# Performance work log

Hardware: AMD Instinct MI355X
Metric: run time of the kernel (lower is better)

Reference implementation:

```python
import jax, jax.numpy as jnp
import numpy as np

N = 50000
E = 800000
F_IN = 128
HID = 128
OUT = 64
EPS = 1e-5


def gcn_conv(x, src, dst, deg_inv_sqrt, W, b):
    # h = x @ W  (dense transform first, like PyG GCNConv)
    h = x @ W  # [N, F_out]
    norm = deg_inv_sqrt[src] * deg_inv_sqrt[dst]  # [E+N] (self-loops included)
    msgs = norm[:, None] * h[src]  # gather + scale, [E+N, F_out]
    out = jax.ops.segment_sum(msgs, dst, num_segments=N)  # scatter-add to targets
    return out + b


def setup_inputs() -> dict:
    key = jax.random.key(0)
    ks = jax.random.split(key, 9)
    x = jax.random.normal(ks[0], (N, F_IN), dtype=jnp.float32)
    edge_index = jax.random.randint(ks[1], (2, E), 0, N, dtype=jnp.int64)
    s = 1.0 / np.sqrt(F_IN)
    W1 = jax.random.uniform(ks[2], (F_IN, HID), jnp.float32, -s, s)
    b1 = jnp.zeros((HID,), jnp.float32)
    sh = 1.0 / np.sqrt(HID)
    Wmu = jax.random.uniform(ks[3], (HID, OUT), jnp.float32, -sh, sh)
    bmu = jnp.zeros((OUT,), jnp.float32)
    Wlv = jax.random.uniform(ks[4], (HID, OUT), jnp.float32, -sh, sh)
    blv = jnp.zeros((OUT,), jnp.float32)
    gamma = jnp.ones((HID,), jnp.float32)
    beta = jnp.zeros((HID,), jnp.float32)
    return {"x": x, "edge_index": edge_index, "W1": W1, "b1": b1,
            "gamma": gamma, "beta": beta, "Wmu": Wmu, "bmu": bmu,
            "Wlv": Wlv, "blv": blv}


def reference(x, edge_index, W1, b1, gamma, beta, Wmu, bmu, Wlv, blv):
    # Add self-loops (GCNConv default) and compute symmetric normalization once.
    loop = jnp.arange(N, dtype=edge_index.dtype)
    src = jnp.concatenate([edge_index[0], loop])
    dst = jnp.concatenate([edge_index[1], loop])
    deg = jax.ops.segment_sum(jnp.ones_like(dst, dtype=x.dtype), dst, num_segments=N)
    deg_inv_sqrt = jnp.where(deg > 0, jax.lax.rsqrt(deg), 0.0)

    h = jax.nn.relu(gcn_conv(x, src, dst, deg_inv_sqrt, W1, b1))
    # per-node LayerNorm over feature dim
    mean = jnp.mean(h, axis=-1, keepdims=True)
    var = jnp.var(h, axis=-1, keepdims=True)
    h = (h - mean) * jax.lax.rsqrt(var + EPS) * gamma + beta

    mu = gcn_conv(h, src, dst, deg_inv_sqrt, Wmu, bmu)
    logvar = gcn_conv(h, src, dst, deg_inv_sqrt, Wlv, blv)
    return mu, logvar
```

## Files before the change

### kernel.cpp

```cpp
#include <hip/hip_runtime.h>

#define NN 50000
#define EE 800000
#define FF 128
#define OO 64
#define EPSF 1e-5f
#define SCB 196
#define EBLK 3125
#define GBLK 391

typedef unsigned int uint;
typedef unsigned short ushort;
typedef __attribute__((ext_vector_type(8))) short short8;
typedef __attribute__((ext_vector_type(4))) float f32x4;

__device__ __forceinline__ float bflo(uint v) { return __uint_as_float(v << 16); }
__device__ __forceinline__ float bfhi(uint v) { return __uint_as_float(v & 0xFFFF0000u); }
__device__ __forceinline__ uint f2bf(float f) {
  uint b = __float_as_uint(f);
  return (b + 0x7FFFu + ((b >> 16) & 1u)) >> 16;
}
__device__ __forceinline__ uint pack2(float x, float y) { return f2bf(x) | (f2bf(y) << 16); }

__device__ __forceinline__ int eidx(const void* ei, long long pos, int f64) {
  if (f64) return (int)((const long long*)ei)[pos];
  return ((const int*)ei)[pos];
}

__global__ void k_init(const void* ei, int* flag, int* cnt) {
  int i = blockIdx.x * 256 + threadIdx.x;
  if (i < NN) cnt[i] = 0;
  if (i == 0) {
    const int* p = (const int*)ei;
    int any = 0;
    for (int j = 1; j < 128; j += 2) any |= p[j];
    *flag = (any == 0) ? 1 : 0;
  }
}

__global__ void k_deg_rank(const void* ei, const int* __restrict__ flag,
                           int* __restrict__ cnt, int* __restrict__ rank) {
  int e = blockIdx.x * 256 + threadIdx.x;
  if (e >= EE) return;
  int f64 = *flag;
  int d = eidx(ei, (long long)EE + e, f64);
  rank[e] = atomicAdd(&cnt[d], 1);
}

__global__ __launch_bounds__(256) void k_dis_part(const int* __restrict__ cnt,
                                                  float* __restrict__ dis,
                                                  int* __restrict__ bsum) {
  int i = blockIdx.x * 256 + threadIdx.x;
  int v = (i < NN) ? cnt[i] : 0;
  if (i < NN) dis[i] = rsqrtf((float)(v + 1));
  int s = v;
#pragma unroll
  for (int m = 1; m < 64; m <<= 1) s += __shfl_xor(s, m);
  __shared__ int ws[4];
  if ((threadIdx.x & 63) == 0) ws[threadIdx.x >> 6] = s;
  __syncthreads();
  if (threadIdx.x == 0) bsum[blockIdx.x] = ws[0] + ws[1] + ws[2] + ws[3];
}

__global__ __launch_bounds__(256) void k_scan_tops(const int* __restrict__ bsum,
                                                   int* __restrict__ boff,
                                                   int* __restrict__ rowptr) {
  __shared__ int s[256];
  int tid = threadIdx.x;
  int v = (tid < SCB) ? bsum[tid] : 0;
  s[tid] = v;
  __syncthreads();
  for (int off = 1; off < 256; off <<= 1) {
    int t = (tid >= off) ? s[tid - off] : 0;
    __syncthreads();
    s[tid] += t;
    __syncthreads();
  }
  if (tid < SCB) boff[tid] = s[tid] - v;
  if (tid == 255) rowptr[NN] = s[255];
}

__global__ __launch_bounds__(256) void k_scan_write(const int* __restrict__ cnt,
                                                    const int* __restrict__ boff,
                                                    int* __restrict__ rowptr) {
  int blk = blockIdx.x, tid = threadIdx.x;
  int i = blk * 256 + tid;
  int v = (i < NN) ? cnt[i] : 0;
  int lane = tid & 63, wid = tid >> 6;
  int inc = v;
#pragma unroll
  for (int off = 1; off < 64; off <<= 1) {
    int t = __shfl_up(inc, off);
    if (lane >= off) inc += t;
  }
  __shared__ int wsum[4];
  if (lane == 63) wsum[wid] = inc;
  __syncthreads();
  int wadd = 0;
  for (int wj = 0; wj < wid; ++wj) wadd += wsum[wj];
  int exc = inc - v + wadd + boff[blk];
  if (i < NN) rowptr[i] = exc;
}

__global__ void k_scatter(const void* ei, const int* __restrict__ flag,
                          const float* __restrict__ dis,
                          const int* __restrict__ rowptr,
                          const int* __restrict__ rank,
                          int2* __restrict__ cw) {
  int e = blockIdx.x * 256 + threadIdx.x;
  if (e >= EE) return;
  int f64 = *flag;
  int s = eidx(ei, e, f64);
  int d = eidx(ei, (long long)EE + e, f64);
  int p = rowptr[d] + rank[e];
  int2 v;
  v.x = s;
  v.y = __float_as_int(dis[s] * dis[d]);
  cw[p] = v;
}

__device__ __forceinline__ int wt_idx(int c, int k) {
  return c * 128 + (k ^ ((c & 7) << 3));
}

__global__ __launch_bounds__(256) void k_gemm1(const float* __restrict__ X,
                                               const float* __restrict__ W,
                                               ushort* __restrict__ T) {
  __shared__ ushort Wt[FF * FF];
  for (int i = threadIdx.x; i < FF * FF; i += 256) {
    int k = i >> 7, c = i & 127;
    Wt[wt_idx(c, k)] = (ushort)f2bf(W[i]);
  }
  __syncthreads();
  int l = threadIdx.x & 63, wv = threadIdx.x >> 6;
  int rbase = blockIdx.x * 128 + wv * 32;
  int lr = l & 15, lk = (l >> 4) << 3;
  f32x4 acc[2][8] = {};
#pragma unroll
  for (int kb = 0; kb < 4; ++kb) {
    int kk = kb * 32 + lk;
    short8 a[2];
#pragma unroll
    for (int rt = 0; rt < 2; ++rt) {
      int row = min(rbase + rt * 16 + lr, NN - 1);
      const float4* ap = (const float4*)(X + (size_t)row * FF + kk);
      float4 x0 = ap[0], x1 = ap[1];
      a[rt][0] = (short)f2bf(x0.x); a[rt][1] = (short)f2bf(x0.y);
      a[rt][2] = (short)f2bf(x0.z); a[rt][3] = (short)f2bf(x0.w);
      a[rt][4] = (short)f2bf(x1.x); a[rt][5] = (short)f2bf(x1.y);
      a[rt][6] = (short)f2bf(x1.z); a[rt][7] = (short)f2bf(x1.w);
    }
#pragma unroll
    for (int ct = 0; ct < 8; ++ct) {
      int c = ct * 16 + lr;
      short8 b = *(const short8*)&Wt[wt_idx(c, kk)];
      acc[0][ct] = __builtin_amdgcn_mfma_f32_16x16x32_bf16(a[0], b, acc[0][ct], 0, 0, 0);
      acc[1][ct] = __builtin_amdgcn_mfma_f32_16x16x32_bf16(a[1], b, acc[1][ct], 0, 0, 0);
    }
  }
  int rl = (l >> 4) * 4;
#pragma unroll
  for (int rt = 0; rt < 2; ++rt)
#pragma unroll
    for (int reg = 0; reg < 4; ++reg) {
      int row = rbase + rt * 16 + rl + reg;
      if (row < NN) {
#pragma unroll
        for (int ct = 0; ct < 8; ++ct)
          T[(size_t)row * FF + ct * 16 + lr] = (ushort)f2bf(acc[rt][ct][reg]);
      }
    }
}

__global__ __launch_bounds__(256) void k_gemm2(const ushort* __restrict__ A,
                                               const float* __restrict__ Wmu,
                                               const float* __restrict__ bmu,
                                               const float* __restrict__ Wlv,
                                               const float* __restrict__ blv,
                                               float* __restrict__ out) {
  __shared__ ushort Wt[FF * FF];
  __shared__ float sb[FF];
  for (int i = threadIdx.x; i < FF * FF; i += 256) {
    int k = i >> 7, c = i & 127;
    float v = (c < OO) ? Wmu[k * OO + c] : Wlv[k * OO + (c - OO)];
    Wt[wt_idx(c, k)] = (ushort)f2bf(v);
  }
  if (threadIdx.x < FF)
    sb[threadIdx.x] = (threadIdx.x < OO) ? bmu[threadIdx.x] : blv[threadIdx.x - OO];
  __syncthreads();
  int l = threadIdx.x & 63, wv = threadIdx.x >> 6;
  int rbase = blockIdx.x * 128 + wv * 32;
  int lr = l & 15, lk = (l >> 4) << 3;
  f32x4 acc[2][8] = {};
#pragma unroll
  for (int kb = 0; kb < 4; ++kb) {
    int kk = kb * 32 + lk;
    short8 a[2];
#pragma unroll
    for (int rt = 0; rt < 2; ++rt) {
      int row = min(rbase + rt * 16 + lr, NN - 1);
      a[rt] = *(const short8*)(A + (size_t)row * FF + kk);
    }
#pragma unroll
    for (int ct = 0; ct < 8; ++ct) {
      int c = ct * 16 + lr;
      short8 b = *(const short8*)&Wt[wt_idx(c, kk)];
      acc[0][ct] = __builtin_amdgcn_mfma_f32_16x16x32_bf16(a[0], b, acc[0][ct], 0, 0, 0);
      acc[1][ct] = __builtin_amdgcn_mfma_f32_16x16x32_bf16(a[1], b, acc[1][ct], 0, 0, 0);
    }
  }
  int rl = (l >> 4) * 4;
#pragma unroll
  for (int rt = 0; rt < 2; ++rt)
#pragma unroll
    for (int reg = 0; reg < 4; ++reg) {
      int row = rbase + rt * 16 + rl + reg;
      if (row < NN) {
#pragma unroll
        for (int ct = 0; ct < 8; ++ct) {
          int c = ct * 16 + lr;
          float v = acc[rt][ct][reg] + sb[c];
          if (ct < 4) out[(size_t)row * OO + c] = v;
          else out[(size_t)NN * OO + (size_t)row * OO + (c - OO)] = v;
        }
      }
    }
}

template <int LN>
__global__ __launch_bounds__(256) void k_gather(const int* __restrict__ rowptr,
                                                const int2* __restrict__ cw,
                                                const float* __restrict__ dis,
                                                const ushort* __restrict__ feat,
                                                const float* __restrict__ b1,
                                                const float* __restrict__ gamma,
                                                const float* __restrict__ beta,
                                                ushort* __restrict__ outp) {
  int gw = (blockIdx.x * 256 + threadIdx.x) >> 6;
  int nw = (gridDim.x * 256) >> 6;
  int lane = threadIdx.x & 63;
  for (int node = gw; node < NN; node += nw) {
    float di = dis[node];
    float sw = di * di;
    uint sv = ((const uint*)(feat + ((size_t)node << 7)))[lane];
    float ax = sw * bflo(sv), ay = sw * bfhi(sv);
    int e = rowptr[node], end = rowptr[node + 1];
    while (end - e >= 16) {
      int2 c[16];
      uint v[16];
#pragma unroll
      for (int j = 0; j < 16; ++j) c[j] = cw[e + j];
#pragma unroll
      for (int j = 0; j < 16; ++j) v[j] = ((const uint*)(feat + ((size_t)c[j].x << 7)))[lane];
#pragma unroll
      for (int j = 0; j < 16; ++j) {
        float wj = __int_as_float(c[j].y);
        ax = fmaf(wj, bflo(v[j]), ax); ay = fmaf(wj, bfhi(v[j]), ay);
      }
      e += 16;
    }
    if (end - e >= 8) {
      int2 c[8];
      uint v[8];
#pragma unroll
      for (int j = 0; j < 8; ++j) c[j] = cw[e + j];
#pragma unroll
      for (int j = 0; j < 8; ++j) v[j] = ((const uint*)(feat + ((size_t)c[j].x << 7)))[lane];
#pragma unroll
      for (int j = 0; j < 8; ++j) {
        float wj = __int_as_float(c[j].y);
        ax = fmaf(wj, bflo(v[j]), ax); ay = fmaf(wj, bfhi(v[j]), ay);
      }
      e += 8;
    }
    if (end - e >= 4) {
      int2 c[4];
      uint v[4];
#pragma unroll
      for (int j = 0; j < 4; ++j) c[j] = cw[e + j];
#pragma unroll
      for (int j = 0; j < 4; ++j) v[j] = ((const uint*)(feat + ((size_t)c[j].x << 7)))[lane];
#pragma unroll
      for (int j = 0; j < 4; ++j) {
        float wj = __int_as_float(c[j].y);
        ax = fmaf(wj, bflo(v[j]), ax); ay = fmaf(wj, bfhi(v[j]), ay);
      }
      e += 4;
    }
    for (; e < end; ++e) {
      int2 c0 = cw[e];
      uint v0 = ((const uint*)(feat + ((size_t)c0.x << 7)))[lane];
      float w0 = __int_as_float(c0.y);
      ax = fmaf(w0, bflo(v0), ax); ay = fmaf(w0, bfhi(v0), ay);
    }
    float ox, oy;
    if (LN) {
      float b0 = b1[2 * lane], b1v = b1[2 * lane + 1];
      float a0 = fmaxf(ax + b0, 0.f);
      float a1 = fmaxf(ay + b1v, 0.f);
      float s = a0 + a1, sq = a0 * a0 + a1 * a1;
#pragma unroll
      for (int m = 1; m < 64; m <<= 1) {
        s += __shfl_xor(s, m);
        sq += __shfl_xor(sq, m);
      }
      float mean = s * (1.f / 128.f);
      float var = sq * (1.f / 128.f) - mean * mean;
      float rstd = rsqrtf(var + EPSF);
      float g0 = gamma[2 * lane], g1 = gamma[2 * lane + 1];
      float be0 = beta[2 * lane], be1 = beta[2 * lane + 1];
      ox = (a0 - mean) * rstd * g0 + be0;
      oy = (a1 - mean) * rstd * g1 + be1;
    } else {
      ox = ax; oy = ay;
    }
    ((uint*)(outp + ((size_t)node << 7)))[lane] = pack2(ox, oy);
  }
}

extern "C" void kernel_launch(void* const* d_in, const int* in_sizes, int n_in,
                              void* d_out, int out_size, void* d_ws, size_t ws_size,
                              hipStream_t stream) {
  const float* x     = (const float*)d_in[0];
  const void*  ei    = d_in[1];
  const float* W1    = (const float*)d_in[2];
  const float* b1    = (const float*)d_in[3];
  const float* gamma = (const float*)d_in[4];
  const float* beta  = (const float*)d_in[5];
  const float* Wmu   = (const float*)d_in[6];
  const float* bmu   = (const float*)d_in[7];
  const float* Wlv   = (const float*)d_in[8];
  const float* blv   = (const float*)d_in[9];
  float* out = (float*)d_out;

  int*   flag   = (int*)d_ws;
  int*   cnt    = flag + 64;
  int*   rowptr = cnt + NN;
  float* dis    = (float*)(rowptr + (NN + 16));
  int*   bsum   = (int*)(dis + NN);
  int*   boff   = bsum + 256;
  int*   rank   = boff + 256;
  size_t off32  = (size_t)(64 + NN + (NN + 16) + NN + 256 + 256 + EE);
  off32 = (off32 + 63) & ~(size_t)63;
  int2*  cw     = (int2*)((int*)d_ws + off32);
  ushort* t  = (ushort*)(cw + EE);
  ushort* h  = t + (size_t)NN * FF;
  ushort* t2 = h + (size_t)NN * FF;

  k_init<<<SCB, 256, 0, stream>>>(ei, flag, cnt);
  k_deg_rank<<<EBLK, 256, 0, stream>>>(ei, flag, cnt, rank);
  k_dis_part<<<SCB, 256, 0, stream>>>(cnt, dis, bsum);
  k_scan_tops<<<1, 256, 0, stream>>>(bsum, boff, rowptr);
  k_scan_write<<<SCB, 256, 0, stream>>>(cnt, boff, rowptr);
  k_scatter<<<EBLK, 256, 0, stream>>>(ei, flag, dis, rowptr, rank, cw);

  k_gemm1<<<GBLK, 256, 0, stream>>>(x, W1, t);
  k_gather<1><<<2048, 256, 0, stream>>>(rowptr, cw, dis, t, b1, gamma, beta, h);
  k_gather<0><<<2048, 256, 0, stream>>>(rowptr, cw, dis, h, b1, gamma, beta, t2);
  k_gemm2<<<GBLK, 256, 0, stream>>>(t2, Wmu, bmu, Wlv, blv, out);
}
```

Baseline: 178.5 us.

## Split each wavefront into four edge groups with 16-byte feature loads in gather

The gather kernel now gives each wavefront one node and splits its 64 lanes into four groups of 16. Each group handles a different edge and each lane loads 16 bytes (8 bf16 features), so the per-edge rows come in as wide vector loads and several edges are in flight at once. The partial sums are combined across groups with cross-lane shuffles. The LayerNorm reduction now runs within 16 lanes, and the launch becomes one node per wave with no grid-stride loop. The cost is extra shuffle work, 8 accumulators per lane, and only two edges per group per iteration instead of the old 16-deep unroll.

New measurement: 165.9 us. 1.08x faster.

```diff
diff --git a/kernel.cpp b/kernel.cpp
--- a/kernel.cpp
+++ b/kernel.cpp
@@ -236,85 +236,95 @@
                                                 const float* __restrict__ gamma,
                                                 const float* __restrict__ beta,
                                                 ushort* __restrict__ outp) {
-  int gw = (blockIdx.x * 256 + threadIdx.x) >> 6;
-  int nw = (gridDim.x * 256) >> 6;
-  int lane = threadIdx.x & 63;
-  for (int node = gw; node < NN; node += nw) {
+  int node = blockIdx.x * 4 + (threadIdx.x >> 6);
+  if (node >= NN) return;
+  int l = threadIdx.x & 63;
+  int g = l >> 4;
+  int c16 = l & 15;
+
+  float acc[8] = {};
+  int e0 = rowptr[node], nE = rowptr[node + 1] - e0;
+  int base = 0;
+  for (; base + 8 <= nE; base += 8) {
+    int2 cA = cw[e0 + base + g];
+    int2 cB = cw[e0 + base + 4 + g];
+    uint4 vA = ((const uint4*)(feat + ((size_t)cA.x << 7)))[c16];
+    uint4 vB = ((const uint4*)(feat + ((size_t)cB.x << 7)))[c16];
+    float wA = __int_as_float(cA.y), wB = __int_as_float(cB.y);
+    acc[0] = fmaf(wA, bflo(vA.x), acc[0]); acc[1] = fmaf(wA, bfhi(vA.x), acc[1]);
+    acc[2] = fmaf(wA, bflo(vA.y), acc[2]); acc[3] = fmaf(wA, bfhi(vA.y), acc[3]);
+    acc[4] = fmaf(wA, bflo(vA.z), acc[4]); acc[5] = fmaf(wA, bfhi(vA.z), acc[5]);
+    acc[6] = fmaf(wA, bflo(vA.w), acc[6]); acc[7] = fmaf(wA, bfhi(vA.w), acc[7]);
+    acc[0] = fmaf(wB, bflo(vB.x), acc[0]); acc[1] = fmaf(wB, bfhi(vB.x), acc[1]);
+    acc[2] = fmaf(wB, bflo(vB.y), acc[2]); acc[3] = fmaf(wB, bfhi(vB.y), acc[3]);
+    acc[4] = fmaf(wB, bflo(vB.z), acc[4]); acc[5] = fmaf(wB, bfhi(vB.z), acc[5]);
+    acc[6] = fmaf(wB, bflo(vB.w), acc[6]); acc[7] = fmaf(wB, bfhi(vB.w), acc[7]);
+  }
+#pragma unroll
+  for (int t = 0; t < 2; ++t) {
+    int idx = base + t * 4 + g;
+    if (idx < nE) {
+      int2 c0 = cw[e0 + idx];
+      uint4 v = ((const uint4*)(feat + ((size_t)c0.x << 7)))[c16];
+      float w0 = __int_as_float(c0.y);
+      acc[0] = fmaf(w0, bflo(v.x), acc[0]); acc[1] = fmaf(w0, bfhi(v.x), acc[1]);
+      acc[2] = fmaf(w0, bflo(v.y), acc[2]); acc[3] = fmaf(w0, bfhi(v.y), acc[3]);
+      acc[4] = fmaf(w0, bflo(v.z), acc[4]); acc[5] = fmaf(w0, bfhi(v.z), acc[5]);
+      acc[6] = fmaf(w0, bflo(v.w), acc[6]); acc[7] = fmaf(w0, bfhi(v.w), acc[7]);
+    }
+  }
+#pragma unroll
+  for (int j = 0; j < 8; ++j) {
+    acc[j] += __shfl_xor(acc[j], 16);
+    acc[j] += __shfl_xor(acc[j], 32);
+  }
+  {
     float di = dis[node];
     float sw = di * di;
-    uint sv = ((const uint*)(feat + ((size_t)node << 7)))[lane];
-    float ax = sw * bflo(sv), ay = sw * bfhi(sv);
-    int e = rowptr[node], end = rowptr[node + 1];
-    while (end - e >= 16) {
-      int2 c[16];
-      uint v[16];
-#pragma unroll
-      for (int j = 0; j < 16; ++j) c[j] = cw[e + j];
-#pragma unroll
-      for (int j = 0; j < 16; ++j) v[j] = ((const uint*)(feat + ((size_t)c[j].x << 7)))[lane];
-#pragma unroll
-      for (int j = 0; j < 16; ++j) {
-        float wj = __int_as_float(c[j].y);
-        ax = fmaf(wj, bflo(v[j]), ax); ay = fmaf(wj, bfhi(v[j]), ay);
-      }
-      e += 16;
-    }
-    if (end - e >= 8) {
-      int2 c[8];
-      uint v[8];
-#pragma unroll
-      for (int j = 0; j < 8; ++j) c[j] = cw[e + j];
-#pragma unroll
-      for (int j = 0; j < 8; ++j) v[j] = ((const uint*)(feat + ((size_t)c[j].x << 7)))[lane];
-#pragma unroll
-      for (int j = 0; j < 8; ++j) {
-        float wj = __int_as_float(c[j].y);
-        ax = fmaf(wj, bflo(v[j]), ax); ay = fmaf(wj, bfhi(v[j]), ay);
-      }
-      e += 8;
-    }
-    if (end - e >= 4) {
-      int2 c[4];
-      uint v[4];
-#pragma unroll
-      for (int j = 0; j < 4; ++j) c[j] = cw[e + j];
-#pragma unroll
-      for (int j = 0; j < 4; ++j) v[j] = ((const uint*)(feat + ((size_t)c[j].x << 7)))[lane];
-#pragma unroll
-      for (int j = 0; j < 4; ++j) {
-        float wj = __int_as_float(c[j].y);
-        ax = fmaf(wj, bflo(v[j]), ax); ay = fmaf(wj, bfhi(v[j]), ay);
-      }
-      e += 4;
-    }
-    for (; e < end; ++e) {
-      int2 c0 = cw[e];
-      uint v0 = ((const uint*)(feat + ((size_t)c0.x << 7)))[lane];
-      float w0 = __int_as_float(c0.y);
-      ax = fmaf(w0, bflo(v0), ax); ay = fmaf(w0, bfhi(v0), ay);
-    }
-    float ox, oy;
-    if (LN) {
-      float b0 = b1[2 * lane], b1v = b1[2 * lane + 1];
-      float a0 = fmaxf(ax + b0, 0.f);
-      float a1 = fmaxf(ay + b1v, 0.f);
-      float s = a0 + a1, sq = a0 * a0 + a1 * a1;
-#pragma unroll
-      for (int m = 1; m < 64; m <<= 1) {
-        s += __shfl_xor(s, m);
-        sq += __shfl_xor(sq, m);
-      }
-      float mean = s * (1.f / 128.f);
-      float var = sq * (1.f / 128.f) - mean * mean;
-      float rstd = rsqrtf(var + EPSF);
-      float g0 = gamma[2 * lane], g1 = gamma[2 * lane + 1];
-      float be0 = beta[2 * lane], be1 = beta[2 * lane + 1];
-      ox = (a0 - mean) * rstd * g0 + be0;
-      oy = (a1 - mean) * rstd * g1 + be1;
-    } else {
-      ox = ax; oy = ay;
-    }
-    ((uint*)(outp + ((size_t)node << 7)))[lane] = pack2(ox, oy);
+    uint4 v = ((const uint4*)(feat + ((size_t)node << 7)))[c16];
+    acc[0] = fmaf(sw, bflo(v.x), acc[0]); acc[1] = fmaf(sw, bfhi(v.x), acc[1]);
+    acc[2] = fmaf(sw, bflo(v.y), acc[2]); acc[3] = fmaf(sw, bfhi(v.y), acc[3]);
+    acc[4] = fmaf(sw, bflo(v.z), acc[4]); acc[5] = fmaf(sw, bfhi(v.z), acc[5]);
+    acc[6] = fmaf(sw, bflo(v.w), acc[6]); acc[7] = fmaf(sw, bfhi(v.w), acc[7]);
+  }
+  int cOff = c16 * 8;
+  float o[8];
+  if (LN) {
+    float4 ba = *(const float4*)&b1[cOff];
+    float4 bb = *(const float4*)&b1[cOff + 4];
+    float a[8];
+    a[0] = fmaxf(acc[0] + ba.x, 0.f); a[1] = fmaxf(acc[1] + ba.y, 0.f);
+    a[2] = fmaxf(acc[2] + ba.z, 0.f); a[3] = fmaxf(acc[3] + ba.w, 0.f);
+    a[4] = fmaxf(acc[4] + bb.x, 0.f); a[5] = fmaxf(acc[5] + bb.y, 0.f);
+    a[6] = fmaxf(acc[6] + bb.z, 0.f); a[7] = fmaxf(acc[7] + bb.w, 0.f);
+    float s = 0.f, sq = 0.f;
+#pragma unroll
+    for (int j = 0; j < 8; ++j) { s += a[j]; sq += a[j] * a[j]; }
+#pragma unroll
+    for (int m = 1; m < 16; m <<= 1) {
+      s += __shfl_xor(s, m);
+      sq += __shfl_xor(sq, m);
+    }
+    float mean = s * (1.f / 128.f);
+    float var = sq * (1.f / 128.f) - mean * mean;
+    float rstd = rsqrtf(var + EPSF);
+    float4 ga = *(const float4*)&gamma[cOff];
+    float4 gb = *(const float4*)&gamma[cOff + 4];
+    float4 ea = *(const float4*)&beta[cOff];
+    float4 eb = *(const float4*)&beta[cOff + 4];
+    o[0] = (a[0] - mean) * rstd * ga.x + ea.x; o[1] = (a[1] - mean) * rstd * ga.y + ea.y;
+    o[2] = (a[2] - mean) * rstd * ga.z + ea.z; o[3] = (a[3] - mean) * rstd * ga.w + ea.w;
+    o[4] = (a[4] - mean) * rstd * gb.x + eb.x; o[5] = (a[5] - mean) * rstd * gb.y + eb.y;
+    o[6] = (a[6] - mean) * rstd * gb.z + eb.z; o[7] = (a[7] - mean) * rstd * gb.w + eb.w;
+  } else {
+#pragma unroll
+    for (int j = 0; j < 8; ++j) o[j] = acc[j];
+  }
+  if (g == 0) {
+    uint4 p;
+    p.x = pack2(o[0], o[1]); p.y = pack2(o[2], o[3]);
+    p.z = pack2(o[4], o[5]); p.w = pack2(o[6], o[7]);
+    ((uint4*)(outp + ((size_t)node << 7)))[c16] = p;
   }
 }
 
@@ -355,7 +365,7 @@
   k_scatter<<<EBLK, 256, 0, stream>>>(ei, flag, dis, rowptr, rank, cw);
 
   k_gemm1<<<GBLK, 256, 0, stream>>>(x, W1, t);
-  k_gather<1><<<2048, 256, 0, stream>>>(rowptr, cw, dis, t, b1, gamma, beta, h);
-  k_gather<0><<<2048, 256, 0, stream>>>(rowptr, cw, dis, h, b1, gamma, beta, t2);
+  k_gather<1><<<(NN + 3) / 4, 256, 0, stream>>>(rowptr, cw, dis, t, b1, gamma, beta, h);
+  k_gather<0><<<(NN + 3) / 4, 256, 0, stream>>>(rowptr, cw, dis, h, b1, gamma, beta, t2);
   k_gemm2<<<GBLK, 256, 0, stream>>>(t2, Wmu, bmu, Wlv, blv, out);
 }
```
